# Kernel tuning notes

Measured on AMD Instinct MI355X. Metric: run time of the kernel, lower is better.

## Reference

```python
import jax, jax.numpy as jnp
import numpy as np

DIM = 64
TIME_DIM = 16
LABEL_DIM = 32
N_HEADS = 4
B = 524288


def _mha(seq, w_in, b_in, w_out, b_out, n_heads=N_HEADS):
    # seq: [B, S, E]; faithful nn.MultiheadAttention (batch_first) self-attention
    Bs, S, E = seq.shape
    D = E // n_heads
    qkv = seq @ w_in + b_in  # [B, S, 3E]
    q, k, v = jnp.split(qkv, 3, axis=-1)
    q = q.reshape(Bs, S, n_heads, D)
    k = k.reshape(Bs, S, n_heads, D)
    v = v.reshape(Bs, S, n_heads, D)
    scale = 1.0 / jnp.sqrt(jnp.asarray(D, seq.dtype))
    scores = jnp.einsum('bshd,bthd->bhst', q, k) * scale
    attn = jax.nn.softmax(scores, axis=-1)
    o = jnp.einsum('bhst,bthd->bshd', attn, v).reshape(Bs, S, E)
    return o @ w_out + b_out


def setup_inputs() -> dict:
    key = jax.random.key(0)
    ks = iter(jax.random.split(key, 64))

    def p(shape):
        return jax.random.normal(next(ks), shape, dtype=jnp.float32) * 0.05

    inp = {
        'x': jax.random.normal(next(ks), (B, DIM), dtype=jnp.float32),
        't': jax.random.uniform(next(ks), (B, 1), dtype=jnp.float32),
        'y': jax.random.normal(next(ks), (B, 40), dtype=jnp.float32),
        # label_proj: Linear(40,32) -> ReLU -> Linear(32,64)
        'lp_w1': p((40, LABEL_DIM)), 'lp_b1': p((LABEL_DIM,)),
        'lp_w2': p((LABEL_DIM, DIM)), 'lp_b2': p((DIM,)),
        # two MultiheadAttention layers (packed in_proj, out_proj)
        'a1_win': p((DIM, 3 * DIM)), 'a1_bin': p((3 * DIM,)),
        'a1_wout': p((DIM, DIM)), 'a1_bout': p((DIM,)),
        'a2_win': p((DIM, 3 * DIM)), 'a2_bin': p((3 * DIM,)),
        'a2_wout': p((DIM, DIM)), 'a2_bout': p((DIM,)),
        # FiLM layers: gamma/beta Linear(dim, dim)
        'f1_gw': p((DIM, DIM)), 'f1_gb': p((DIM,)),
        'f1_bw': p((DIM, DIM)), 'f1_bb': p((DIM,)),
        'f2_gw': p((DIM, DIM)), 'f2_gb': p((DIM,)),
        'f2_bw': p((DIM, DIM)), 'f2_bb': p((DIM,)),
        # block1: Linear(80,64)->ReLU->Linear(64,64); block2/3: Linear(64,64)x2
        'b1_w1': p((DIM + TIME_DIM, DIM)), 'b1_b1': p((DIM,)),
        'b1_w2': p((DIM, DIM)), 'b1_b2': p((DIM,)),
        'b2_w1': p((DIM, DIM)), 'b2_b1': p((DIM,)),
        'b2_w2': p((DIM, DIM)), 'b2_b2': p((DIM,)),
        'b3_w1': p((DIM, DIM)), 'b3_b1': p((DIM,)),
        'b3_w2': p((DIM, DIM)), 'b3_b2': p((DIM,)),
        'out_w': p((DIM, DIM)), 'out_b': p((DIM,)),
    }
    return inp


def reference(x, t, y,
              lp_w1, lp_b1, lp_w2, lp_b2,
              a1_win, a1_bin, a1_wout, a1_bout,
              a2_win, a2_bin, a2_wout, a2_bout,
              f1_gw, f1_gb, f1_bw, f1_bb,
              f2_gw, f2_gb, f2_bw, f2_bb,
              b1_w1, b1_b1, b1_w2, b1_b2,
              b2_w1, b2_b1, b2_w2, b2_b2,
              b3_w1, b3_b1, b3_w2, b3_b2,
              out_w, out_b):
    half = TIME_DIM // 2
    freq = (2.0 ** jnp.arange(half, dtype=x.dtype)) * jnp.pi  # [8]
    args = t * freq[None, :]                                   # [B, 8]
    t_feats = jnp.concatenate([jnp.sin(args), jnp.cos(args)], axis=-1)  # [B, 16]

    h = jnp.concatenate([x, t_feats], axis=-1)                 # [B, 80]
    h = jax.nn.relu(h @ b1_w1 + b1_b1) @ b1_w2 + b1_b2         # block1

    y_embed = jax.nn.relu(y @ lp_w1 + lp_b1) @ lp_w2 + lp_b2   # [B, 64]

    seq = jnp.stack([h, y_embed], axis=1)                      # [B, 2, 64]
    h = _mha(seq, a1_win, a1_bin, a1_wout, a1_bout)[:, 0]
    h = (y_embed @ f1_gw + f1_gb) * h + (y_embed @ f1_bw + f1_bb)  # FiLM1
    h = h + (jax.nn.relu(h @ b2_w1 + b2_b1) @ b2_w2 + b2_b2)   # block2 + residual

    seq = jnp.stack([h, y_embed], axis=1)
    h = _mha(seq, a2_win, a2_bin, a2_wout, a2_bout)[:, 0]
    h = (y_embed @ f2_gw + f2_gb) * h + (y_embed @ f2_bw + f2_bb)  # FiLM2
    h = h + (jax.nn.relu(h @ b3_w1 + b3_b1) @ b3_w2 + b3_b2)   # block3 + residual

    return h @ out_w + out_b
```

## Files before the change

kernel.cpp:

```cpp
#include <hip/hip_runtime.h>
#include <math.h>

typedef __attribute__((ext_vector_type(8))) short   short8;
typedef __attribute__((ext_vector_type(8))) _Float16 half8;
typedef __attribute__((ext_vector_type(2))) __fp16  fp16x2;
typedef __attribute__((ext_vector_type(4))) float   f32x4;

__device__ __forceinline__ half8 as_h8(short8 s) {
  union { short8 s; half8 h; } u; u.s = s; return u.h;
}
#define MFMA16(a,b,c) __builtin_amdgcn_mfma_f32_16x16x32_f16(as_h8(a), as_h8(b), (c), 0, 0, 0)

#define WS_B1W1   0
#define WS_B1W2   12
#define WS_LPW1   20
#define WS_BIAS   24
#define WS_A1WIN  28
#define WS_A1WOUT 52
#define WS_B2W1   76
#define WS_B2W2   84
#define WS_A2WIN  92
#define WS_A2WOUT 116
#define WS_B3W1   140
#define WS_B3W2   148
#define WS_OUTW   156
#define WS_COMP   164
#define WS_FRAGS  196

__device__ __forceinline__ unsigned short f2h(float f) {
  union { _Float16 h; unsigned short u; } r;
  r.h = (_Float16)f;
  return r.u;
}
__device__ __forceinline__ unsigned int pkrtz(float lo, float hi) {
  union { fp16x2 h; unsigned int u; } r;
  r.h = __builtin_amdgcn_cvt_pkrtz(lo, hi);
  return r.u;
}
__device__ __forceinline__ float h_lo(unsigned int p) {
  union { unsigned short s; _Float16 h; } c; c.s = (unsigned short)p; return (float)c.h;
}
__device__ __forceinline__ float h_hi(unsigned int p) {
  union { unsigned short s; _Float16 h; } c; c.s = (unsigned short)(p >> 16); return (float)c.h;
}

__device__ __forceinline__ short8 pack8(float4 a, float4 b) {
  union { unsigned int u[4]; short8 s; } r;
  r.u[0] = pkrtz(a.x, a.y);
  r.u[1] = pkrtz(a.z, a.w);
  r.u[2] = pkrtz(b.x, b.y);
  r.u[3] = pkrtz(b.z, b.w);
  return r.s;
}

__device__ __forceinline__ short8 zero8() {
  short8 r;
  #pragma unroll
  for (int j = 0; j < 8; ++j) r[j] = 0;
  return r;
}

__device__ __forceinline__ f32x4 relu4(f32x4 v) {
  f32x4 r;
  #pragma unroll
  for (int j = 0; j < 4; ++j) r[j] = fmaxf(v[j], 0.0f);
  return r;
}

__global__ __launch_bounds__(64) void prep_kernel(
    const float* b1w1, const float* b1w2, const float* lpw1, const float* lpw2,
    const float* a1win, const float* a1wout, const float* f1gw, const float* f1bw,
    const float* b2w1, const float* b2w2, const float* a2win, const float* a2wout,
    const float* f2gw, const float* f2bw, const float* b3w1, const float* b3w2,
    const float* outw, unsigned short* ws)
{
  const float* WS_[17] = {b1w1,b1w2,lpw1,lpw2,a1win,a1wout,f1gw,f1bw,b2w1,b2w2,
                          a2win,a2wout,f2gw,f2bw,b3w1,b3w2,outw};
  const int KA[17] = {80,64,40,32,64,64,64,64,64,64,64,64,64,64,64,64,64};
  const int NA[17] = {64,64,32,64,192,64,64,64,64,64,192,64,64,64,64,64,64};
  const int FO[17] = {0,12,20,24,28,52,60,68,76,84,92,116,124,132,140,148,156};

  const int b = blockIdx.x;
  int m = 0;
  #pragma unroll
  for (int i = 1; i < 17; ++i) if (b >= FO[i]) m = i;
  const int f  = b - FO[m];
  const int K  = KA[m], N = NA[m];
  const int kc = (K + 31) >> 5;
  const int n  = f / kc, c = f % kc;

  const int lane = threadIdx.x;
  const int col  = n * 16 + (lane & 15);
  const int kb   = c * 32 + ((lane >> 4) * 8);
  const float* W = WS_[m];

  short8 r;
  #pragma unroll
  for (int j = 0; j < 8; ++j) {
    const int k = kb + j;
    const float v = (k < K) ? W[(size_t)k * N + col] : 0.0f;
    r[j] = (short)f2h(v);
  }
  *reinterpret_cast<short8*>(ws + (size_t)b * 512 + lane * 8) = r;
}

__global__ __launch_bounds__(64) void prep2_kernel(
    const float* lpw2, const float* lpb2,
    const float* a1win, const float* a1bin, const float* a2win, const float* a2bin,
    const float* f1gw, const float* f1gb, const float* f1bw, const float* f1bb,
    const float* f2gw, const float* f2gb, const float* f2bw, const float* f2bb,
    unsigned short* ws)
{
  const int b = blockIdx.x, lane = threadIdx.x;
  if (b < 32) {
    const int cm = b >> 2, n = b & 3;
    const float* W; int ldw, colOff; float sgn = 1.0f;
    switch (cm) {
      case 0:  W = a1win; ldw = 192; colOff = 64;  sgn = -1.0f; break;
      case 1:  W = a1win; ldw = 192; colOff = 128; break;
      case 2:  W = f1gw;  ldw = 64;  colOff = 0;   break;
      case 3:  W = f1bw;  ldw = 64;  colOff = 0;   break;
      case 4:  W = a2win; ldw = 192; colOff = 64;  sgn = -1.0f; break;
      case 5:  W = a2win; ldw = 192; colOff = 128; break;
      case 6:  W = f2gw;  ldw = 64;  colOff = 0;   break;
      default: W = f2bw;  ldw = 64;  colOff = 0;   break;
    }
    const int col = colOff + n * 16 + (lane & 15);
    const int kb  = (lane >> 4) * 8;
    short8 r;
    #pragma unroll
    for (int j = 0; j < 8; ++j) {
      const int k = kb + j;
      float acc = 0.0f;
      for (int m = 0; m < 64; ++m) acc += lpw2[k * 64 + m] * W[(size_t)m * ldw + col];
      r[j] = (short)f2h(sgn * acc);
    }
    *reinterpret_cast<short8*>(ws + (size_t)(WS_COMP + b) * 512 + lane * 8) = r;
  } else {
    const int vb = b - 32;
    const int rep = vb >> 2, which = vb & 3;
    const float* win = rep ? a2win : a1win;
    const float* bin = rep ? a2bin : a1bin;
    const float* W; int ldw, colOff; const float* bias0 = nullptr; float sgn = 1.0f;
    switch (which) {
      case 0:  W = win; ldw = 192; colOff = 64;  sgn = -1.0f; break;
      case 1:  W = win; ldw = 192; colOff = 128; bias0 = bin + 128; break;
      case 2:  W = rep ? f2gw : f1gw; ldw = 64; colOff = 0; bias0 = rep ? f2gb : f1gb; break;
      default: W = rep ? f2bw : f1bw; ldw = 64; colOff = 0; bias0 = rep ? f2bb : f1bb; break;
    }
    const int c = lane;
    float acc = 0.0f;
    for (int m = 0; m < 64; ++m) acc += lpb2[m] * W[(size_t)m * ldw + colOff + c];
    acc *= sgn;
    if (bias0) acc += bias0[c];
    float* wsb = reinterpret_cast<float*>(ws + WS_BIAS * 512);
    wsb[rep * 256 + which * 64 + c] = acc;
  }
}

__device__ __forceinline__ short8 ldA(const unsigned short* Ab, int c) {
  return *reinterpret_cast<const short8*>(Ab + c * 32);
}
__device__ __forceinline__ void stC_pk(unsigned short* Cb, int n, unsigned int p01, unsigned int p23) {
  unsigned short* p = Cb + n * 16;
  p[0]   = (unsigned short)p01;
  p[72]  = (unsigned short)(p01 >> 16);
  p[144] = (unsigned short)p23;
  p[216] = (unsigned short)(p23 >> 16);
}
__device__ __forceinline__ void stC(unsigned short* Cb, int n, f32x4 v) {
  stC_pk(Cb, n, pkrtz(v[0], v[1]), pkrtz(v[2], v[3]));
}
__device__ __forceinline__ float rowsum16(float v) {
  float r = v;
  r += __int_as_float(__builtin_amdgcn_update_dpp(
        __float_as_int(r), __float_as_int(r), 0x128, 0xf, 0xf, false));
  r += __int_as_float(__builtin_amdgcn_update_dpp(
        __float_as_int(r), __float_as_int(r), 0x124, 0xf, 0xf, false));
  r += __int_as_float(__builtin_amdgcn_update_dpp(
        __float_as_int(r), __float_as_int(r), 0x122, 0xf, 0xf, false));
  r += __int_as_float(__builtin_amdgcn_update_dpp(
        __float_as_int(r), __float_as_int(r), 0x121, 0xf, 0xf, false));
  return r;
}

__global__ __launch_bounds__(256, 4) void flow_mfma(
    const float* __restrict__ x, const float* __restrict__ t, const float* __restrict__ y,
    const float* __restrict__ b1b1, const float* __restrict__ b1b2,
    const float* __restrict__ lpb1,
    const float* __restrict__ a1bin, const float* __restrict__ a1bout,
    const float* __restrict__ a2bin, const float* __restrict__ a2bout,
    const float* __restrict__ b2b1, const float* __restrict__ b2b2,
    const float* __restrict__ b3b1, const float* __restrict__ b3b2,
    const float* __restrict__ outb,
    const unsigned short* __restrict__ ws,
    float* __restrict__ out, int Btotal)
{
  __shared__ __align__(16) unsigned short lds[4][2 * 16 * 72];
  const int tid  = threadIdx.x;
  const int lane = tid & 63, wid = tid >> 6;
  const int lrow = lane & 15, grp = lane >> 4;
  const int r0   = (blockIdx.x * 4 + wid) * 32;
  if (r0 >= Btotal) return;
  unsigned short* T = &lds[wid][0];
  unsigned short* Ab[2];
  unsigned short* Cb[2];
  #pragma unroll
  for (int u = 0; u < 2; ++u) {
    Ab[u] = T + u * 1152 + lrow * 72 + grp * 8;
    Cb[u] = T + u * 1152 + grp * 288 + lrow;
  }
  const short8* wsl = reinterpret_cast<const short8*>(ws) + lane;
  const float*  wsb = reinterpret_cast<const float*>(ws + WS_BIAS * 512);

  short8 hA0[2], hA1[2];
  {
    short8 tF[2];
    #pragma unroll
    for (int u = 0; u < 2; ++u) {
      const size_t row = (size_t)r0 + u * 16 + lrow;
      const float4* xp = reinterpret_cast<const float4*>(x + row * 64) + grp * 2;
      hA0[u] = pack8(xp[0], xp[1]);
      hA1[u] = pack8(xp[8], xp[9]);
      const float tv = t[row];
      float s = __sinf(3.14159265358979323846f * tv);
      float c = __cosf(3.14159265358979323846f * tv);
      short8 hp;
      #pragma unroll
      for (int j = 0; j < 8; ++j) {
        const float v = (grp == 0) ? s : ((grp == 1) ? c : 0.0f);
        hp[j] = (short)f2h(v);
        const float s2 = 2.0f * s * c;
        const float c2 = 1.0f - 2.0f * s * s;
        s = s2; c = c2;
      }
      tF[u] = hp;
    }
    #pragma unroll
    for (int n = 0; n < 4; ++n) {
      const short8 B0 = wsl[(WS_B1W1 + n * 3 + 0) * 64];
      const short8 B1 = wsl[(WS_B1W1 + n * 3 + 1) * 64];
      const short8 B2 = wsl[(WS_B1W1 + n * 3 + 2) * 64];
      const float bias = b1b1[n * 16 + lrow];
      #pragma unroll
      for (int u = 0; u < 2; ++u) {
        f32x4 acc = {bias, bias, bias, bias};
        acc = MFMA16(hA0[u], B0, acc);
        acc = MFMA16(hA1[u], B1, acc);
        acc = MFMA16(tF[u],  B2, acc);
        stC(Cb[u], n, relu4(acc));
      }
    }
  }
  #pragma unroll
  for (int u = 0; u < 2; ++u) { hA0[u] = ldA(Ab[u], 0); hA1[u] = ldA(Ab[u], 1); }
  #pragma unroll
  for (int n = 0; n < 4; ++n) {
    const short8 B0 = wsl[(WS_B1W2 + n * 2 + 0) * 64];
    const short8 B1 = wsl[(WS_B1W2 + n * 2 + 1) * 64];
    const float bias = b1b2[n * 16 + lrow];
    #pragma unroll
    for (int u = 0; u < 2; ++u) {
      f32x4 acc = {bias, bias, bias, bias};
      acc = MFMA16(hA0[u], B0, acc);
      acc = MFMA16(hA1[u], B1, acc);
      stC(Cb[u], n, acc);
    }
  }
  #pragma unroll
  for (int u = 0; u < 2; ++u) { hA0[u] = ldA(Ab[u], 0); hA1[u] = ldA(Ab[u], 1); }

  short8 zA[2];
  {
    short8 y0[2], y1[2];
    #pragma unroll
    for (int u = 0; u < 2; ++u) {
      const float* yrow = y + ((size_t)r0 + u * 16 + lrow) * 40;
      y0[u] = pack8(*reinterpret_cast<const float4*>(yrow + grp * 8),
                    *reinterpret_cast<const float4*>(yrow + grp * 8 + 4));
      y1[u] = (grp == 0) ? pack8(*reinterpret_cast<const float4*>(yrow + 32),
                                 *reinterpret_cast<const float4*>(yrow + 36))
                         : zero8();
    }
    #pragma unroll
    for (int n = 0; n < 2; ++n) {
      const short8 B0 = wsl[(WS_LPW1 + n * 2 + 0) * 64];
      const short8 B1 = wsl[(WS_LPW1 + n * 2 + 1) * 64];
      const float bias = lpb1[n * 16 + lrow];
      #pragma unroll
      for (int u = 0; u < 2; ++u) {
        f32x4 acc = {bias, bias, bias, bias};
        acc = MFMA16(y0[u], B0, acc);
        acc = MFMA16(y1[u], B1, acc);
        stC(Cb[u], n, relu4(acc));
      }
    }
    #pragma unroll
    for (int u = 0; u < 2; ++u) zA[u] = ldA(Ab[u], 0);
  }

  unsigned int hCp01[4][2], hCp23[4][2];
  #pragma unroll 1
  for (int rep = 0; rep < 2; ++rep) {
    const int WIN  = rep ? WS_A2WIN  : WS_A1WIN;
    const int WOUT = rep ? WS_A2WOUT : WS_A1WOUT;
    const int CK   = WS_COMP + rep * 16;
    const int CV   = WS_COMP + rep * 16 + 4;
    const int CG   = WS_COMP + rep * 16 + 8;
    const int CB   = WS_COMP + rep * 16 + 12;
    const int W1   = rep ? WS_B3W1   : WS_B2W1;
    const int W2   = rep ? WS_B3W2   : WS_B2W2;
    const float* binp  = rep ? a2bin  : a1bin;
    const float* boutp = rep ? a2bout : a1bout;
    const float* w1b   = rep ? b3b1   : b2b1;
    const float* w2b   = rep ? b3b2   : b2b2;
    const float* bcomp = wsb + rep * 256;

    #pragma unroll
    for (int n = 0; n < 4; ++n) {
      float pr[2][4];
      {
        const short8 Bq0 = wsl[(WIN + n * 2 + 0) * 64];
        const short8 Bq1 = wsl[(WIN + n * 2 + 1) * 64];
        const short8 Bk0 = wsl[(WIN + (4 + n) * 2 + 0) * 64];
        const short8 Bk1 = wsl[(WIN + (4 + n) * 2 + 1) * 64];
        const short8 BCK = wsl[(CK + n) * 64];
        const float bq = binp[n * 16 + lrow];
        const float ck = bcomp[n * 16 + lrow];
        #pragma unroll
        for (int u = 0; u < 2; ++u) {
          f32x4 q = {bq, bq, bq, bq};
          q = MFMA16(hA0[u], Bq0, q);
          q = MFMA16(hA1[u], Bq1, q);
          f32x4 kd = {ck, ck, ck, ck};
          kd = MFMA16(hA0[u], Bk0, kd);
          kd = MFMA16(hA1[u], Bk1, kd);
          kd = MFMA16(zA[u],  BCK, kd);
          #pragma unroll
          for (int j = 0; j < 4; ++j) {
            const float d = rowsum16(q[j] * kd[j]);
            pr[u][j] = 1.0f / (1.0f + __expf(-0.25f * d));
          }
        }
      }
      {
        const short8 Bv0 = wsl[(WIN + (8 + n) * 2 + 0) * 64];
        const short8 Bv1 = wsl[(WIN + (8 + n) * 2 + 1) * 64];
        const short8 BCV = wsl[(CV + n) * 64];
        const float bv  = binp[128 + n * 16 + lrow];
        const float bvp = bcomp[64 + n * 16 + lrow];
        #pragma unroll
        for (int u = 0; u < 2; ++u) {
          f32x4 v0 = {bv, bv, bv, bv};
          v0 = MFMA16(hA0[u], Bv0, v0);
          v0 = MFMA16(hA1[u], Bv1, v0);
          f32x4 v1 = {bvp, bvp, bvp, bvp};
          v1 = MFMA16(zA[u], BCV, v1);
          f32x4 ov;
          #pragma unroll
          for (int j = 0; j < 4; ++j) ov[j] = fmaf(pr[u][j], v0[j] - v1[j], v1[j]);
          stC(Cb[u], n, ov);
        }
      }
    }
    #pragma unroll
    for (int u = 0; u < 2; ++u) { hA0[u] = ldA(Ab[u], 0); hA1[u] = ldA(Ab[u], 1); }

    #pragma unroll
    for (int n = 0; n < 4; ++n) {
      f32x4 at[2];
      {
        const short8 Bo0 = wsl[(WOUT + n * 2 + 0) * 64];
        const short8 Bo1 = wsl[(WOUT + n * 2 + 1) * 64];
        const float bo = boutp[n * 16 + lrow];
        #pragma unroll
        for (int u = 0; u < 2; ++u) {
          at[u] = (f32x4){bo, bo, bo, bo};
          at[u] = MFMA16(hA0[u], Bo0, at[u]);
          at[u] = MFMA16(hA1[u], Bo1, at[u]);
        }
      }
      {
        const short8 BG = wsl[(CG + n) * 64];
        const short8 BB = wsl[(CB + n) * 64];
        const float gp  = bcomp[128 + n * 16 + lrow];
        const float fbp = bcomp[192 + n * 16 + lrow];
        #pragma unroll
        for (int u = 0; u < 2; ++u) {
          f32x4 g = {gp, gp, gp, gp};
          g = MFMA16(zA[u], BG, g);
          f32x4 fb = {fbp, fbp, fbp, fbp};
          fb = MFMA16(zA[u], BB, fb);
          f32x4 hv;
          #pragma unroll
          for (int j = 0; j < 4; ++j) hv[j] = fmaf(g[j], at[u][j], fb[j]);
          const unsigned int p01 = pkrtz(hv[0], hv[1]);
          const unsigned int p23 = pkrtz(hv[2], hv[3]);
          hCp01[n][u] = p01; hCp23[n][u] = p23;
          stC_pk(Cb[u], n, p01, p23);
        }
      }
    }
    #pragma unroll
    for (int u = 0; u < 2; ++u) { hA0[u] = ldA(Ab[u], 0); hA1[u] = ldA(Ab[u], 1); }

    #pragma unroll
    for (int n = 0; n < 4; ++n) {
      const short8 B0 = wsl[(W1 + n * 2 + 0) * 64];
      const short8 B1 = wsl[(W1 + n * 2 + 1) * 64];
      const float bias = w1b[n * 16 + lrow];
      #pragma unroll
      for (int u = 0; u < 2; ++u) {
        f32x4 acc = {bias, bias, bias, bias};
        acc = MFMA16(hA0[u], B0, acc);
        acc = MFMA16(hA1[u], B1, acc);
        stC(Cb[u], n, relu4(acc));
      }
    }
    #pragma unroll
    for (int u = 0; u < 2; ++u) { hA0[u] = ldA(Ab[u], 0); hA1[u] = ldA(Ab[u], 1); }
    #pragma unroll
    for (int n = 0; n < 4; ++n) {
      const short8 B0 = wsl[(W2 + n * 2 + 0) * 64];
      const short8 B1 = wsl[(W2 + n * 2 + 1) * 64];
      const float bias = w2b[n * 16 + lrow];
      #pragma unroll
      for (int u = 0; u < 2; ++u) {
        f32x4 acc = {bias, bias, bias, bias};
        acc = MFMA16(hA0[u], B0, acc);
        acc = MFMA16(hA1[u], B1, acc);
        acc[0] += h_lo(hCp01[n][u]);
        acc[1] += h_hi(hCp01[n][u]);
        acc[2] += h_lo(hCp23[n][u]);
        acc[3] += h_hi(hCp23[n][u]);
        stC(Cb[u], n, acc);
      }
    }
    #pragma unroll
    for (int u = 0; u < 2; ++u) { hA0[u] = ldA(Ab[u], 0); hA1[u] = ldA(Ab[u], 1); }
  }

  #pragma unroll
  for (int n = 0; n < 4; ++n) {
    const short8 B0 = wsl[(WS_OUTW + n * 2 + 0) * 64];
    const short8 B1 = wsl[(WS_OUTW + n * 2 + 1) * 64];
    const float bias = outb[n * 16 + lrow];
    #pragma unroll
    for (int u = 0; u < 2; ++u) {
      f32x4 a = {bias, bias, bias, bias};
      a = MFMA16(hA0[u], B0, a);
      a = MFMA16(hA1[u], B1, a);
      float* ob = out + ((size_t)r0 + u * 16 + grp * 4) * 64 + n * 16 + lrow;
      #pragma unroll
      for (int j = 0; j < 4; ++j)
        ob[j * 64] = a[j];
    }
  }
}

extern "C" void kernel_launch(void* const* d_in, const int* in_sizes, int n_in,
                              void* d_out, int out_size, void* d_ws, size_t ws_size,
                              hipStream_t stream) {
  (void)n_in; (void)out_size; (void)ws_size;
  const float* p[37];
  for (int i = 0; i < 37; ++i) p[i] = (const float*)d_in[i];
  unsigned short* ws = (unsigned short*)d_ws;

  prep_kernel<<<dim3(164), dim3(64), 0, stream>>>(
      p[23], p[25], p[3], p[5], p[7], p[9], p[15], p[17],
      p[27], p[29], p[11], p[13], p[19], p[21], p[31], p[33], p[35], ws);

  prep2_kernel<<<dim3(40), dim3(64), 0, stream>>>(
      p[5],  p[6],
      p[7],  p[8],  p[11], p[12],
      p[15], p[16], p[17], p[18],
      p[19], p[20], p[21], p[22],
      ws);

  const int B = in_sizes[0] / 64;
  const int grid = (B + 127) / 128;
  flow_mfma<<<dim3(grid), dim3(256), 0, stream>>>(
      p[0], p[1], p[2],
      p[24], p[26],
      p[4],
      p[8],  p[10],
      p[12], p[14],
      p[28], p[30],
      p[32], p[34],
      p[36],
      ws, (float*)d_out, B);
}
```

Measured before the change: 202.0 us.

## Process three 16-row tiles per wave and fuse attention loops

```diff
diff --git a/kernel.cpp b/kernel.cpp
--- a/kernel.cpp
+++ b/kernel.cpp
@@ -1,5 +1,7 @@
 #include <hip/hip_runtime.h>
 #include <math.h>
+
+#define NU 3
 
 typedef __attribute__((ext_vector_type(8))) short   short8;
 typedef __attribute__((ext_vector_type(8))) _Float16 half8;
@@ -196,29 +198,33 @@
     const unsigned short* __restrict__ ws,
     float* __restrict__ out, int Btotal)
 {
-  __shared__ __align__(16) unsigned short lds[4][2 * 16 * 72];
+  __shared__ __align__(16) unsigned short lds[4][NU * 16 * 72];
   const int tid  = threadIdx.x;
   const int lane = tid & 63, wid = tid >> 6;
   const int lrow = lane & 15, grp = lane >> 4;
-  const int r0   = (blockIdx.x * 4 + wid) * 32;
+  const int r0   = (blockIdx.x * 4 + wid) * (NU * 16);
   if (r0 >= Btotal) return;
   unsigned short* T = &lds[wid][0];
-  unsigned short* Ab[2];
-  unsigned short* Cb[2];
-  #pragma unroll
-  for (int u = 0; u < 2; ++u) {
+  unsigned short* Ab[NU];
+  unsigned short* Cb[NU];
+  bool act[NU];
+  int rbase[NU];
+  #pragma unroll
+  for (int u = 0; u < NU; ++u) {
     Ab[u] = T + u * 1152 + lrow * 72 + grp * 8;
     Cb[u] = T + u * 1152 + grp * 288 + lrow;
+    act[u]   = (r0 + u * 16) < Btotal;
+    rbase[u] = act[u] ? (r0 + u * 16) : (Btotal - 16);
   }
   const short8* wsl = reinterpret_cast<const short8*>(ws) + lane;
   const float*  wsb = reinterpret_cast<const float*>(ws + WS_BIAS * 512);
 
-  short8 hA0[2], hA1[2];
+  short8 hA0[NU], hA1[NU];
   {
-    short8 tF[2];
-    #pragma unroll
-    for (int u = 0; u < 2; ++u) {
-      const size_t row = (size_t)r0 + u * 16 + lrow;
+    short8 tF[NU];
+    #pragma unroll
+    for (int u = 0; u < NU; ++u) {
+      const size_t row = (size_t)rbase[u] + lrow;
       const float4* xp = reinterpret_cast<const float4*>(x + row * 64) + grp * 2;
       hA0[u] = pack8(xp[0], xp[1]);
       hA1[u] = pack8(xp[8], xp[9]);
@@ -243,7 +249,7 @@
       const short8 B2 = wsl[(WS_B1W1 + n * 3 + 2) * 64];
       const float bias = b1b1[n * 16 + lrow];
       #pragma unroll
-      for (int u = 0; u < 2; ++u) {
+      for (int u = 0; u < NU; ++u) {
         f32x4 acc = {bias, bias, bias, bias};
         acc = MFMA16(hA0[u], B0, acc);
         acc = MFMA16(hA1[u], B1, acc);
@@ -253,14 +259,14 @@
     }
   }
   #pragma unroll
-  for (int u = 0; u < 2; ++u) { hA0[u] = ldA(Ab[u], 0); hA1[u] = ldA(Ab[u], 1); }
+  for (int u = 0; u < NU; ++u) { hA0[u] = ldA(Ab[u], 0); hA1[u] = ldA(Ab[u], 1); }
   #pragma unroll
   for (int n = 0; n < 4; ++n) {
     const short8 B0 = wsl[(WS_B1W2 + n * 2 + 0) * 64];
     const short8 B1 = wsl[(WS_B1W2 + n * 2 + 1) * 64];
     const float bias = b1b2[n * 16 + lrow];
     #pragma unroll
-    for (int u = 0; u < 2; ++u) {
+    for (int u = 0; u < NU; ++u) {
       f32x4 acc = {bias, bias, bias, bias};
       acc = MFMA16(hA0[u], B0, acc);
       acc = MFMA16(hA1[u], B1, acc);
@@ -268,14 +274,14 @@
     }
   }
   #pragma unroll
-  for (int u = 0; u < 2; ++u) { hA0[u] = ldA(Ab[u], 0); hA1[u] = ldA(Ab[u], 1); }
-
-  short8 zA[2];
+  for (int u = 0; u < NU; ++u) { hA0[u] = ldA(Ab[u], 0); hA1[u] = ldA(Ab[u], 1); }
+
+  short8 zA[NU];
   {
-    short8 y0[2], y1[2];
-    #pragma unroll
-    for (int u = 0; u < 2; ++u) {
-      const float* yrow = y + ((size_t)r0 + u * 16 + lrow) * 40;
+    short8 y0[NU], y1[NU];
+    #pragma unroll
+    for (int u = 0; u < NU; ++u) {
+      const float* yrow = y + ((size_t)rbase[u] + lrow) * 40;
       y0[u] = pack8(*reinterpret_cast<const float4*>(yrow + grp * 8),
                     *reinterpret_cast<const float4*>(yrow + grp * 8 + 4));
       y1[u] = (grp == 0) ? pack8(*reinterpret_cast<const float4*>(yrow + 32),
@@ -288,7 +294,7 @@
       const short8 B1 = wsl[(WS_LPW1 + n * 2 + 1) * 64];
       const float bias = lpb1[n * 16 + lrow];
       #pragma unroll
-      for (int u = 0; u < 2; ++u) {
+      for (int u = 0; u < NU; ++u) {
         f32x4 acc = {bias, bias, bias, bias};
         acc = MFMA16(y0[u], B0, acc);
         acc = MFMA16(y1[u], B1, acc);
@@ -296,10 +302,10 @@
       }
     }
     #pragma unroll
-    for (int u = 0; u < 2; ++u) zA[u] = ldA(Ab[u], 0);
-  }
-
-  unsigned int hCp01[4][2], hCp23[4][2];
+    for (int u = 0; u < NU; ++u) zA[u] = ldA(Ab[u], 0);
+  }
+
+  unsigned int hCp01[4][NU], hCp23[4][NU];
   #pragma unroll 1
   for (int rep = 0; rep < 2; ++rep) {
     const int WIN  = rep ? WS_A2WIN  : WS_A1WIN;
@@ -316,93 +322,76 @@
     const float* w2b   = rep ? b3b2   : b2b2;
     const float* bcomp = wsb + rep * 256;
 
-    #pragma unroll
+    #pragma unroll 1
     for (int n = 0; n < 4; ++n) {
-      float pr[2][4];
-      {
-        const short8 Bq0 = wsl[(WIN + n * 2 + 0) * 64];
-        const short8 Bq1 = wsl[(WIN + n * 2 + 1) * 64];
-        const short8 Bk0 = wsl[(WIN + (4 + n) * 2 + 0) * 64];
-        const short8 Bk1 = wsl[(WIN + (4 + n) * 2 + 1) * 64];
-        const short8 BCK = wsl[(CK + n) * 64];
-        const float bq = binp[n * 16 + lrow];
-        const float ck = bcomp[n * 16 + lrow];
+      const short8 Bq0 = wsl[(WIN + n * 2 + 0) * 64];
+      const short8 Bq1 = wsl[(WIN + n * 2 + 1) * 64];
+      const short8 Bk0 = wsl[(WIN + (4 + n) * 2 + 0) * 64];
+      const short8 Bk1 = wsl[(WIN + (4 + n) * 2 + 1) * 64];
+      const short8 BCK = wsl[(CK + n) * 64];
+      const short8 Bv0 = wsl[(WIN + (8 + n) * 2 + 0) * 64];
+      const short8 Bv1 = wsl[(WIN + (8 + n) * 2 + 1) * 64];
+      const short8 BCV = wsl[(CV + n) * 64];
+      const float bq  = binp[n * 16 + lrow];
+      const float ck  = bcomp[n * 16 + lrow];
+      const float bv  = binp[128 + n * 16 + lrow];
+      const float bvp = bcomp[64 + n * 16 + lrow];
+      #pragma unroll
+      for (int u = 0; u < NU; ++u) {
+        f32x4 q = {bq, bq, bq, bq};
+        q = MFMA16(hA0[u], Bq0, q);
+        q = MFMA16(hA1[u], Bq1, q);
+        f32x4 kd = {ck, ck, ck, ck};
+        kd = MFMA16(hA0[u], Bk0, kd);
+        kd = MFMA16(hA1[u], Bk1, kd);
+        kd = MFMA16(zA[u],  BCK, kd);
+        f32x4 v0 = {bv, bv, bv, bv};
+        v0 = MFMA16(hA0[u], Bv0, v0);
+        v0 = MFMA16(hA1[u], Bv1, v0);
+        f32x4 v1 = {bvp, bvp, bvp, bvp};
+        v1 = MFMA16(zA[u], BCV, v1);
+        f32x4 ov;
         #pragma unroll
-        for (int u = 0; u < 2; ++u) {
-          f32x4 q = {bq, bq, bq, bq};
-          q = MFMA16(hA0[u], Bq0, q);
-          q = MFMA16(hA1[u], Bq1, q);
-          f32x4 kd = {ck, ck, ck, ck};
-          kd = MFMA16(hA0[u], Bk0, kd);
-          kd = MFMA16(hA1[u], Bk1, kd);
-          kd = MFMA16(zA[u],  BCK, kd);
-          #pragma unroll
-          for (int j = 0; j < 4; ++j) {
-            const float d = rowsum16(q[j] * kd[j]);
-            pr[u][j] = 1.0f / (1.0f + __expf(-0.25f * d));
-          }
+        for (int j = 0; j < 4; ++j) {
+          const float d = rowsum16(q[j] * kd[j]);
+          const float p0 = 1.0f / (1.0f + __expf(-0.25f * d));
+          ov[j] = fmaf(p0, v0[j] - v1[j], v1[j]);
         }
-      }
-      {
-        const short8 Bv0 = wsl[(WIN + (8 + n) * 2 + 0) * 64];
-        const short8 Bv1 = wsl[(WIN + (8 + n) * 2 + 1) * 64];
-        const short8 BCV = wsl[(CV + n) * 64];
-        const float bv  = binp[128 + n * 16 + lrow];
-        const float bvp = bcomp[64 + n * 16 + lrow];
+        stC(Cb[u], n, ov);
+      }
+    }
+    #pragma unroll
+    for (int u = 0; u < NU; ++u) { hA0[u] = ldA(Ab[u], 0); hA1[u] = ldA(Ab[u], 1); }
+
+    #pragma unroll
+    for (int n = 0; n < 4; ++n) {
+      const short8 Bo0 = wsl[(WOUT + n * 2 + 0) * 64];
+      const short8 Bo1 = wsl[(WOUT + n * 2 + 1) * 64];
+      const short8 BG  = wsl[(CG + n) * 64];
+      const short8 BB  = wsl[(CB + n) * 64];
+      const float bo  = boutp[n * 16 + lrow];
+      const float gp  = bcomp[128 + n * 16 + lrow];
+      const float fbp = bcomp[192 + n * 16 + lrow];
+      #pragma unroll
+      for (int u = 0; u < NU; ++u) {
+        f32x4 at = {bo, bo, bo, bo};
+        at = MFMA16(hA0[u], Bo0, at);
+        at = MFMA16(hA1[u], Bo1, at);
+        f32x4 g = {gp, gp, gp, gp};
+        g = MFMA16(zA[u], BG, g);
+        f32x4 fb = {fbp, fbp, fbp, fbp};
+        fb = MFMA16(zA[u], BB, fb);
+        f32x4 hv;
         #pragma unroll
-        for (int u = 0; u < 2; ++u) {
-          f32x4 v0 = {bv, bv, bv, bv};
-          v0 = MFMA16(hA0[u], Bv0, v0);
-          v0 = MFMA16(hA1[u], Bv1, v0);
-          f32x4 v1 = {bvp, bvp, bvp, bvp};
-          v1 = MFMA16(zA[u], BCV, v1);
-          f32x4 ov;
-          #pragma unroll
-          for (int j = 0; j < 4; ++j) ov[j] = fmaf(pr[u][j], v0[j] - v1[j], v1[j]);
-          stC(Cb[u], n, ov);
-        }
-      }
-    }
-    #pragma unroll
-    for (int u = 0; u < 2; ++u) { hA0[u] = ldA(Ab[u], 0); hA1[u] = ldA(Ab[u], 1); }
-
-    #pragma unroll
-    for (int n = 0; n < 4; ++n) {
-      f32x4 at[2];
-      {
-        const short8 Bo0 = wsl[(WOUT + n * 2 + 0) * 64];
-        const short8 Bo1 = wsl[(WOUT + n * 2 + 1) * 64];
-        const float bo = boutp[n * 16 + lrow];
-        #pragma unroll
-        for (int u = 0; u < 2; ++u) {
-          at[u] = (f32x4){bo, bo, bo, bo};
-          at[u] = MFMA16(hA0[u], Bo0, at[u]);
-          at[u] = MFMA16(hA1[u], Bo1, at[u]);
-        }
-      }
-      {
-        const short8 BG = wsl[(CG + n) * 64];
-        const short8 BB = wsl[(CB + n) * 64];
-        const float gp  = bcomp[128 + n * 16 + lrow];
-        const float fbp = bcomp[192 + n * 16 + lrow];
-        #pragma unroll
-        for (int u = 0; u < 2; ++u) {
-          f32x4 g = {gp, gp, gp, gp};
-          g = MFMA16(zA[u], BG, g);
-          f32x4 fb = {fbp, fbp, fbp, fbp};
-          fb = MFMA16(zA[u], BB, fb);
-          f32x4 hv;
-          #pragma unroll
-          for (int j = 0; j < 4; ++j) hv[j] = fmaf(g[j], at[u][j], fb[j]);
-          const unsigned int p01 = pkrtz(hv[0], hv[1]);
-          const unsigned int p23 = pkrtz(hv[2], hv[3]);
-          hCp01[n][u] = p01; hCp23[n][u] = p23;
-          stC_pk(Cb[u], n, p01, p23);
-        }
-      }
-    }
-    #pragma unroll
-    for (int u = 0; u < 2; ++u) { hA0[u] = ldA(Ab[u], 0); hA1[u] = ldA(Ab[u], 1); }
+        for (int j = 0; j < 4; ++j) hv[j] = fmaf(g[j], at[j], fb[j]);
+        const unsigned int p01 = pkrtz(hv[0], hv[1]);
+        const unsigned int p23 = pkrtz(hv[2], hv[3]);
+        hCp01[n][u] = p01; hCp23[n][u] = p23;
+        stC_pk(Cb[u], n, p01, p23);
+      }
+    }
+    #pragma unroll
+    for (int u = 0; u < NU; ++u) { hA0[u] = ldA(Ab[u], 0); hA1[u] = ldA(Ab[u], 1); }
 
     #pragma unroll
     for (int n = 0; n < 4; ++n) {
@@ -410,7 +399,7 @@
       const short8 B1 = wsl[(W1 + n * 2 + 1) * 64];
       const float bias = w1b[n * 16 + lrow];
       #pragma unroll
-      for (int u = 0; u < 2; ++u) {
+      for (int u = 0; u < NU; ++u) {
         f32x4 acc = {bias, bias, bias, bias};
         acc = MFMA16(hA0[u], B0, acc);
         acc = MFMA16(hA1[u], B1, acc);
@@ -418,14 +407,14 @@
       }
     }
     #pragma unroll
-    for (int u = 0; u < 2; ++u) { hA0[u] = ldA(Ab[u], 0); hA1[u] = ldA(Ab[u], 1); }
+    for (int u = 0; u < NU; ++u) { hA0[u] = ldA(Ab[u], 0); hA1[u] = ldA(Ab[u], 1); }
     #pragma unroll
     for (int n = 0; n < 4; ++n) {
       const short8 B0 = wsl[(W2 + n * 2 + 0) * 64];
       const short8 B1 = wsl[(W2 + n * 2 + 1) * 64];
       const float bias = w2b[n * 16 + lrow];
       #pragma unroll
-      for (int u = 0; u < 2; ++u) {
+      for (int u = 0; u < NU; ++u) {
         f32x4 acc = {bias, bias, bias, bias};
         acc = MFMA16(hA0[u], B0, acc);
         acc = MFMA16(hA1[u], B1, acc);
@@ -437,23 +426,25 @@
       }
     }
     #pragma unroll
-    for (int u = 0; u < 2; ++u) { hA0[u] = ldA(Ab[u], 0); hA1[u] = ldA(Ab[u], 1); }
-  }
-
-  #pragma unroll
+    for (int u = 0; u < NU; ++u) { hA0[u] = ldA(Ab[u], 0); hA1[u] = ldA(Ab[u], 1); }
+  }
+
+  #pragma unroll 1
   for (int n = 0; n < 4; ++n) {
     const short8 B0 = wsl[(WS_OUTW + n * 2 + 0) * 64];
     const short8 B1 = wsl[(WS_OUTW + n * 2 + 1) * 64];
     const float bias = outb[n * 16 + lrow];
     #pragma unroll
-    for (int u = 0; u < 2; ++u) {
+    for (int u = 0; u < NU; ++u) {
       f32x4 a = {bias, bias, bias, bias};
       a = MFMA16(hA0[u], B0, a);
       a = MFMA16(hA1[u], B1, a);
-      float* ob = out + ((size_t)r0 + u * 16 + grp * 4) * 64 + n * 16 + lrow;
-      #pragma unroll
-      for (int j = 0; j < 4; ++j)
-        ob[j * 64] = a[j];
+      if (act[u]) {
+        float* ob = out + ((size_t)rbase[u] + grp * 4) * 64 + n * 16 + lrow;
+        #pragma unroll
+        for (int j = 0; j < 4; ++j)
+          ob[j * 64] = a[j];
+      }
     }
   }
 }
@@ -478,7 +469,8 @@
       ws);
 
   const int B = in_sizes[0] / 64;
-  const int grid = (B + 127) / 128;
+  const int rowsPerBlock = 4 * NU * 16;
+  const int grid = (B + rowsPerBlock - 1) / rowsPerBlock;
   flow_mfma<<<dim3(grid), dim3(256), 0, stream>>>(
       p[0], p[1], p[2],
       p[24], p[26],
```

Result: faster. 187.5 us (-7.2%).
